# Kernel optimization log

Hardware: AMD Instinct MI355X
Metric: run time of the kernel (lower is better)

Reference implementation:

```python
import jax, jax.numpy as jnp
import numpy as np

B, L, D = 4, 2048, 768
H, K = 12, 9
IPG = D // H  # in-channels per group = head_size = 64
PAD = (K - 1) // 2


def setup_inputs() -> dict:
    key = jax.random.key(0)
    ks = jax.random.split(key, 8)
    s = lambda k, shape, scale: jax.random.normal(k, shape, dtype=jnp.float32) * scale
    return {
        "query": s(ks[0], (B, L, D), 1.0),
        "dw_w": s(ks[1], (D, 1, K), 0.1),          # depthwise Conv1d weight, no bias
        "pw_w": s(ks[2], (H, IPG, IPG), 0.05),     # grouped 1x1 conv [head, out_pg, in_pg]
        "pw_b": s(ks[3], (D,), 0.02),
        "ak_w": s(ks[4], (H, K, IPG), 0.05),       # conv_attn_kernel grouped 1x1 [head, K, in_pg]
        "ak_b": s(ks[5], (H * K,), 0.02),
        "pt_w": s(ks[6], (D, D), 0.02),            # conv_attn_point Linear weight [out, in]
        "pt_b": s(ks[7], (D,), 0.02),
    }


def _sdconv(query, dw_w, pw_w, pw_b, ak_w, ak_b, pt_w, pt_b):
    b, l, d = query.shape
    # SeparableConv1d: depthwise conv (groups=D, kernel K, padding PAD, no bias)
    x = query.transpose(0, 2, 1)  # [B, D, L]
    dw = jax.lax.conv_general_dilated(
        x, dw_w, window_strides=(1,), padding=[(PAD, PAD)],
        feature_group_count=d, dimension_numbers=("NCH", "OIH", "NCH"))  # [B, D, L]
    # grouped pointwise conv (groups=H, kernel 1)
    dwg = dw.reshape(b, H, IPG, l)
    pw = jnp.einsum("bhil,hoi->bhol", dwg, pw_w).reshape(b, d, l) + pw_b[None, :, None]
    key_conv_attn = pw.transpose(0, 2, 1)  # [B, L, D]
    # stride == 1 path: elementwise gate with query
    conv_attn = key_conv_attn * query  # [B, L, D]
    # conv_attn_kernel: grouped 1x1 conv D -> H*K (per head: IPG -> K)
    ca = conv_attn.reshape(b, l, H, IPG)
    kern = jnp.einsum("blhi,hki->blhk", ca, ak_w) + ak_b.reshape(H, K)  # [B, L, H, K]
    w = jax.nn.softmax(kern, axis=-1)  # softmax over kernel positions
    # conv_attn_point linear on value (= query here)
    v = query @ pt_w.T + pt_b  # [B, L, D]
    # unfold: local windows of size K around each position
    vp = jnp.pad(v, ((0, 0), (PAD, PAD), (0, 0)))
    idx = jnp.arange(l)[:, None] + jnp.arange(K)[None, :]  # [L, K]
    win = vp[:, idx]  # [B, L, K, D]
    winh = win.reshape(b, l, K, H, IPG)
    out = jnp.einsum("blkhd,blhk->blhd", winh, w).reshape(b, l, d)
    return out


def reference(query, dw_w, pw_w, pw_b, ak_w, ak_b, pt_w, pt_b):
    return _sdconv(query, dw_w, pw_w, pw_b, ak_w, ak_b, pt_w, pt_b)
```

## Files before the change

### kernel.cpp

```cpp
#include <hip/hip_runtime.h>
#include <math.h>

#define NB 4
#define NL 2048
#define ND 768
#define NH 12
#define NK 9
#define NIPG 64
#define NPAD 4
#define MT 112

typedef __attribute__((ext_vector_type(8))) short s16x8;
typedef __attribute__((ext_vector_type(4))) float f32x4;

__device__ __forceinline__ unsigned short f2bf(float f) {
  unsigned int u = __float_as_uint(f);
  unsigned int r = (u + 0x7FFFu + ((u >> 16) & 1u)) >> 16;
  return (unsigned short)r;
}
__device__ __forceinline__ float bf2f(unsigned short s) {
  return __uint_as_float(((unsigned int)s) << 16);
}
__device__ __forceinline__ void gload16(const void* g, void* l) {
  __builtin_amdgcn_global_load_lds((const __attribute__((address_space(1))) void*)g,
                                   (__attribute__((address_space(3))) void*)l,
                                   16, 0, 0);
}

__global__ __launch_bounds__(256) void prep(const float* __restrict__ pt_w,
                                            const float* __restrict__ pw_w,
                                            const float* __restrict__ ak_w,
                                            unsigned short* __restrict__ ptb,
                                            unsigned short* __restrict__ pwb,
                                            unsigned short* __restrict__ akp) {
  const int t = blockIdx.x * 256 + threadIdx.x;
  if (t < ND * ND / 4) {
    float4 f = ((const float4*)pt_w)[t];
    ushort4 o; o.x = f2bf(f.x); o.y = f2bf(f.y); o.z = f2bf(f.z); o.w = f2bf(f.w);
    ((ushort4*)ptb)[t] = o;
  }
  if (t < NH * NIPG * NIPG / 4) {
    float4 f = ((const float4*)pw_w)[t];
    ushort4 o; o.x = f2bf(f.x); o.y = f2bf(f.y); o.z = f2bf(f.z); o.w = f2bf(f.w);
    ((ushort4*)pwb)[t] = o;
  }
  if (t < NH * 16 * NIPG) {
    const int h = t >> 10;
    const int r = t & 1023;
    const int k = r >> 6;
    const int i = r & 63;
    akp[t] = (k < NK) ? f2bf(ak_w[((size_t)h * NK + k) * NIPG + i]) : (unsigned short)0;
  }
}

__global__ __launch_bounds__(256) void attn_w(const float* __restrict__ q,
                                              const float* __restrict__ dw_w,
                                              const unsigned short* __restrict__ pwb,
                                              const float* __restrict__ pw_b,
                                              const unsigned short* __restrict__ akp,
                                              const float* __restrict__ ak_b,
                                              float* __restrict__ wout,
                                              unsigned short* __restrict__ qb) {
  __shared__ float qs[72][68];
  __shared__ unsigned char ab[8192];
  const int l0 = blockIdx.x * 64;
  const int h  = blockIdx.y;
  const int b  = blockIdx.z;
  const int d0 = h * NIPG;
  const int t  = threadIdx.x;
  const int lane = t & 63;
  const int wv = t >> 6;

  {
    const int sl = t >> 4;
    const int sc = (t & 15) * 4;
    for (int r = sl; r < 72; r += 16) {
      const int l = l0 - NPAD + r;
      float4 val = make_float4(0.f, 0.f, 0.f, 0.f);
      if (l >= 0 && l < NL) val = *(const float4*)&q[((size_t)(b * NL + l)) * ND + d0 + sc];
      *(float4*)&qs[r][sc] = val;
      if (r >= NPAD && r < NPAD + 64) {
        ushort4 ub;
        ub.x = f2bf(val.x); ub.y = f2bf(val.y); ub.z = f2bf(val.z); ub.w = f2bf(val.w);
        *(ushort4*)&qb[((size_t)(b * NL + l)) * ND + d0 + sc] = ub;
      }
    }
  }
  float dwk[NK];
#pragma unroll
  for (int k = 0; k < NK; ++k) dwk[k] = dw_w[(size_t)(d0 + lane) * NK + k];
  __syncthreads();

  const int lset = wv * 16;
#pragma unroll
  for (int l2 = 0; l2 < 16; ++l2) {
    const int l = lset + l2;
    float s = 0.f;
#pragma unroll
    for (int k = 0; k < NK; ++k) s = fmaf(qs[l + k][lane], dwk[k], s);
    const int byte = ((l * 64 + lane) * 2) ^ ((l & 7) << 4);
    *(unsigned short*)&ab[byte] = f2bf(s);
  }
  __syncthreads();

  const int fr = lane & 15;
  const int fq = lane >> 4;

  s16x8 av0, av1;
  {
    const int row = lset + fr;
    const int b0 = ((row * 64 + fq * 8) * 2)      ^ ((row & 7) << 4);
    const int b1 = ((row * 64 + 32 + fq * 8) * 2) ^ ((row & 7) << 4);
    av0 = *(const s16x8*)&ab[b0];
    av1 = *(const s16x8*)&ab[b1];
  }
  const unsigned short* pwh = pwb + (size_t)h * NIPG * NIPG;
  f32x4 accp[4];
#pragma unroll
  for (int n = 0; n < 4; ++n) {
    accp[n] = (f32x4){0.f, 0.f, 0.f, 0.f};
    const int o = n * 16 + fr;
    s16x8 bv0 = *(const s16x8*)&pwh[o * 64 + fq * 8];
    s16x8 bv1 = *(const s16x8*)&pwh[o * 64 + 32 + fq * 8];
    accp[n] = __builtin_amdgcn_mfma_f32_16x16x32_bf16(av0, bv0, accp[n], 0, 0, 0);
    accp[n] = __builtin_amdgcn_mfma_f32_16x16x32_bf16(av1, bv1, accp[n], 0, 0, 0);
  }
  __syncthreads();

#pragma unroll
  for (int n = 0; n < 4; ++n) {
    const int o = n * 16 + fr;
    const float pb = pw_b[d0 + o];
#pragma unroll
    for (int j = 0; j < 4; ++j) {
      const int row = lset + fq * 4 + j;
      const float ca = (accp[n][j] + pb) * qs[row + NPAD][o];
      const int byte = ((row * 64 + o) * 2) ^ ((row & 7) << 4);
      *(unsigned short*)&ab[byte] = f2bf(ca);
    }
  }
  __syncthreads();

  f32x4 acck = (f32x4){0.f, 0.f, 0.f, 0.f};
  {
    const int row = lset + fr;
    const int b0 = ((row * 64 + fq * 8) * 2)      ^ ((row & 7) << 4);
    const int b1 = ((row * 64 + 32 + fq * 8) * 2) ^ ((row & 7) << 4);
    s16x8 a0 = *(const s16x8*)&ab[b0];
    s16x8 a1 = *(const s16x8*)&ab[b1];
    const unsigned short* akh = akp + (size_t)h * 16 * NIPG;
    s16x8 b0v = *(const s16x8*)&akh[fr * 64 + fq * 8];
    s16x8 b1v = *(const s16x8*)&akh[fr * 64 + 32 + fq * 8];
    acck = __builtin_amdgcn_mfma_f32_16x16x32_bf16(a0, b0v, acck, 0, 0, 0);
    acck = __builtin_amdgcn_mfma_f32_16x16x32_bf16(a1, b1v, acck, 0, 0, 0);
  }

  const bool kvalid = fr < NK;
  const float akbv = kvalid ? ak_b[h * NK + fr] : 0.f;
#pragma unroll
  for (int j = 0; j < 4; ++j) {
    float val = acck[j] + akbv;
    float mv = kvalid ? val : -3.4e38f;
#pragma unroll
    for (int mm = 1; mm < 16; mm <<= 1) mv = fmaxf(mv, __shfl_xor(mv, mm));
    const float e = kvalid ? __expf(val - mv) : 0.f;
    float ssum = e;
#pragma unroll
    for (int mm = 1; mm < 16; mm <<= 1) ssum += __shfl_xor(ssum, mm);
    if (kvalid) {
      const int row = l0 + lset + fq * 4 + j;
      wout[(((size_t)(b * NL + row)) * NH + h) * NK + fr] = e / ssum;
    }
  }
}

__global__ __launch_bounds__(256) void gemm_conv(const unsigned short* __restrict__ qb,
                                                 const unsigned short* __restrict__ ptb,
                                                 const float* __restrict__ bias,
                                                 const float* __restrict__ w,
                                                 float* __restrict__ out) {
  __shared__ unsigned char lds[33792];
  const int t = threadIdx.x;
  const long mo = (long)blockIdx.x * MT;
  const int n0 = blockIdx.y * 128;
  const int lane = t & 63;
  const int wv = t >> 6;
  const int wr = wv >> 1, wc = wv & 1;
  const int fr = lane & 15;
  const int fq = lane >> 4;

  const int soff = t * 16;
  const int sr = soff >> 6;
  const int scb = soff & 63;
  const unsigned char* gA0 = (const unsigned char*)qb + (mo - 8 + sr) * (long)(ND * 2) + scb;
  const unsigned char* gA1 = gA0 + (long)64 * (ND * 2);
  const unsigned char* gB0 = (const unsigned char*)ptb + (size_t)(n0 + sr) * (ND * 2) + scb;
  const unsigned char* gB1 = gB0 + (size_t)64 * (ND * 2);

  int aoff[4], boff[4];
#pragma unroll
  for (int m = 0; m < 4; ++m)
    aoff[m] = ((wr * 64 + m * 16 + fr) * 32 + fq * 8) * 2;
#pragma unroll
  for (int n = 0; n < 4; ++n)
    boff[n] = 8192 + ((wc * 64 + n * 16 + fr) * 32 + fq * 8) * 2;

#define STAGE(kt, buf)                                             \
  do {                                                             \
    const long kb_ = (long)(kt) * 64;                              \
    unsigned char* base_ = &lds[(buf) * 16384];                    \
    gload16(gA0 + kb_, base_ + soff);                              \
    gload16(gA1 + kb_, base_ + 4096 + soff);                       \
    gload16(gB0 + kb_, base_ + 8192 + soff);                       \
    gload16(gB1 + kb_, base_ + 12288 + soff);                      \
  } while (0)

  f32x4 acc[4][4] = {};
  STAGE(0, 0);
  __syncthreads();
  for (int kt = 0; kt < ND / 32; ++kt) {
    const int cur = kt & 1;
    if (kt + 1 < ND / 32) STAGE(kt + 1, cur ^ 1);
    const unsigned char* bb = &lds[cur * 16384];
    s16x8 av[4], bv[4];
#pragma unroll
    for (int m = 0; m < 4; ++m) av[m] = *(const s16x8*)&bb[aoff[m]];
#pragma unroll
    for (int n = 0; n < 4; ++n) bv[n] = *(const s16x8*)&bb[boff[n]];
#pragma unroll
    for (int m = 0; m < 4; ++m)
#pragma unroll
      for (int n = 0; n < 4; ++n)
        acc[m][n] = __builtin_amdgcn_mfma_f32_16x16x32_bf16(av[m], bv[n], acc[m][n], 0, 0, 0);
    __syncthreads();
  }
#undef STAGE

  unsigned short* vt = (unsigned short*)lds;
#pragma unroll
  for (int m = 0; m < 4; ++m) {
#pragma unroll
    for (int n = 0; n < 4; ++n) {
      const int rb = wr * 64 + m * 16 + fq * 4;
      const int cc = wc * 64 + n * 16 + fr;
      const float bbv = bias[n0 + cc];
#pragma unroll
      for (int j = 0; j < 4; ++j)
        vt[(rb + j) * 132 + cc] = f2bf(acc[m][n][j] + bbv);
    }
  }
  __syncthreads();

  const int cq = (t & 31) * 4;
  const int r0 = 8 + (t >> 5) * 14;
  const int h = (n0 + cq) >> 6;
  float4 win[NK];
#pragma unroll
  for (int k = 0; k < NK; ++k) {
    ushort4 u = *(const ushort4*)&vt[(r0 - 4 + k) * 132 + cq];
    win[k] = make_float4(bf2f(u.x), bf2f(u.y), bf2f(u.z), bf2f(u.w));
  }
#pragma unroll
  for (int i = 0; i < 14; ++i) {
    const int r = r0 + i;
    const long g = mo + r - 8;
    if (g < (long)NB * NL) {
      const int l = (int)(g & (NL - 1));
      const float* wp = &w[((size_t)g * NH + h) * NK];
      float4 a = make_float4(0.f, 0.f, 0.f, 0.f);
#pragma unroll
      for (int k = 0; k < NK; ++k) {
        const int lk = l + k - NPAD;
        if (lk >= 0 && lk < NL) {
          const float wk = wp[k];
          a.x = fmaf(wk, win[k].x, a.x);
          a.y = fmaf(wk, win[k].y, a.y);
          a.z = fmaf(wk, win[k].z, a.z);
          a.w = fmaf(wk, win[k].w, a.w);
        }
      }
      *(float4*)&out[(size_t)g * ND + n0 + cq] = a;
    }
    if (i < 13) {
#pragma unroll
      for (int k = 0; k < NK - 1; ++k) win[k] = win[k + 1];
      ushort4 u = *(const ushort4*)&vt[(r + 5) * 132 + cq];
      win[NK - 1] = make_float4(bf2f(u.x), bf2f(u.y), bf2f(u.z), bf2f(u.w));
    }
  }
}

extern "C" void kernel_launch(void* const* d_in, const int* in_sizes, int n_in,
                              void* d_out, int out_size, void* d_ws, size_t ws_size,
                              hipStream_t stream) {
  const float* query = (const float*)d_in[0];
  const float* dw_w  = (const float*)d_in[1];
  const float* pw_w  = (const float*)d_in[2];
  const float* pw_b  = (const float*)d_in[3];
  const float* ak_w  = (const float*)d_in[4];
  const float* ak_b  = (const float*)d_in[5];
  const float* pt_w  = (const float*)d_in[6];
  const float* pt_b  = (const float*)d_in[7];
  float* out = (float*)d_out;

  float* w = (float*)d_ws;
  unsigned short* qb  = (unsigned short*)(w + (size_t)NB * NL * NH * NK);
  unsigned short* ptb = qb + (size_t)NB * NL * ND;
  unsigned short* pwb = ptb + (size_t)ND * ND;
  unsigned short* akp = pwb + (size_t)NH * NIPG * NIPG;

  prep<<<ND * ND / 4 / 256, 256, 0, stream>>>(pt_w, pw_w, ak_w, ptb, pwb, akp);

  dim3 g2(NL / 64, NH, NB);
  attn_w<<<g2, 256, 0, stream>>>(query, dw_w, pwb, pw_b, akp, ak_b, w, qb);

  dim3 g3((NB * NL + MT - 1) / MT, ND / 128, 1);
  gemm_conv<<<g3, 256, 0, stream>>>(qb, ptb, pt_b, w, out);
}
```

Baseline: 148.4 us.

## Halve GEMM N-tile to 64 and store attn_w query tile as bf16 with sliding window

The fused GEMM+conv kernel now uses a 128x64 output tile instead of 128x128, so each wave computes 32 rows by 64 columns and only half the threads load B. This doubles the grid size and cuts LDS use, which should raise occupancy and wave count across CUs, at the cost of more A-tile reloads. In attn_w the query tile in LDS is kept as bf16 instead of fp32, and the depthwise conv uses a register sliding window to cut LDS reads. The bf16 staging also lowers precision of the depthwise conv and gating inputs.

```diff
diff --git a/kernel.cpp b/kernel.cpp
--- a/kernel.cpp
+++ b/kernel.cpp
@@ -61,7 +61,7 @@
                                               const float* __restrict__ ak_b,
                                               float* __restrict__ wout,
                                               unsigned short* __restrict__ qb) {
-  __shared__ float qs[72][68];
+  __shared__ unsigned short qs[72][68];
   __shared__ unsigned char ab[8192];
   const int l0 = blockIdx.x * 64;
   const int h  = blockIdx.y;
@@ -76,14 +76,14 @@
     const int sc = (t & 15) * 4;
     for (int r = sl; r < 72; r += 16) {
       const int l = l0 - NPAD + r;
-      float4 val = make_float4(0.f, 0.f, 0.f, 0.f);
-      if (l >= 0 && l < NL) val = *(const float4*)&q[((size_t)(b * NL + l)) * ND + d0 + sc];
-      *(float4*)&qs[r][sc] = val;
-      if (r >= NPAD && r < NPAD + 64) {
-        ushort4 ub;
+      ushort4 ub = make_ushort4(0, 0, 0, 0);
+      if (l >= 0 && l < NL) {
+        float4 val = *(const float4*)&q[((size_t)(b * NL + l)) * ND + d0 + sc];
         ub.x = f2bf(val.x); ub.y = f2bf(val.y); ub.z = f2bf(val.z); ub.w = f2bf(val.w);
-        *(ushort4*)&qb[((size_t)(b * NL + l)) * ND + d0 + sc] = ub;
+        if (r >= NPAD && r < NPAD + 64)
+          *(ushort4*)&qb[((size_t)(b * NL + l)) * ND + d0 + sc] = ub;
       }
+      *(ushort4*)&qs[r][sc] = ub;
     }
   }
   float dwk[NK];
@@ -92,14 +92,24 @@
   __syncthreads();
 
   const int lset = wv * 16;
-#pragma unroll
-  for (int l2 = 0; l2 < 16; ++l2) {
-    const int l = lset + l2;
-    float s = 0.f;
-#pragma unroll
-    for (int k = 0; k < NK; ++k) s = fmaf(qs[l + k][lane], dwk[k], s);
-    const int byte = ((l * 64 + lane) * 2) ^ ((l & 7) << 4);
-    *(unsigned short*)&ab[byte] = f2bf(s);
+  {
+    float win9[NK];
+#pragma unroll
+    for (int k = 0; k < NK; ++k) win9[k] = bf2f(qs[lset + k][lane]);
+#pragma unroll
+    for (int l2 = 0; l2 < 16; ++l2) {
+      const int l = lset + l2;
+      float s = 0.f;
+#pragma unroll
+      for (int k = 0; k < NK; ++k) s = fmaf(win9[k], dwk[k], s);
+      const int byte = ((l * 64 + lane) * 2) ^ ((l & 7) << 4);
+      *(unsigned short*)&ab[byte] = f2bf(s);
+      if (l2 < 15) {
+#pragma unroll
+        for (int k = 0; k < NK - 1; ++k) win9[k] = win9[k + 1];
+        win9[NK - 1] = bf2f(qs[lset + l2 + NK][lane]);
+      }
+    }
   }
   __syncthreads();
 
@@ -134,7 +144,7 @@
 #pragma unroll
     for (int j = 0; j < 4; ++j) {
       const int row = lset + fq * 4 + j;
-      const float ca = (accp[n][j] + pb) * qs[row + NPAD][o];
+      const float ca = (accp[n][j] + pb) * bf2f(qs[row + NPAD][o]);
       const int byte = ((row * 64 + o) * 2) ^ ((row & 7) << 4);
       *(unsigned short*)&ab[byte] = f2bf(ca);
     }
@@ -179,13 +189,12 @@
                                                  const float* __restrict__ bias,
                                                  const float* __restrict__ w,
                                                  float* __restrict__ out) {
-  __shared__ unsigned char lds[33792];
+  __shared__ unsigned char lds[24576];
   const int t = threadIdx.x;
   const long mo = (long)blockIdx.x * MT;
-  const int n0 = blockIdx.y * 128;
+  const int n0 = blockIdx.y * 64;
   const int lane = t & 63;
   const int wv = t >> 6;
-  const int wr = wv >> 1, wc = wv & 1;
   const int fr = lane & 15;
   const int fq = lane >> 4;
 
@@ -194,41 +203,39 @@
   const int scb = soff & 63;
   const unsigned char* gA0 = (const unsigned char*)qb + (mo - 8 + sr) * (long)(ND * 2) + scb;
   const unsigned char* gA1 = gA0 + (long)64 * (ND * 2);
-  const unsigned char* gB0 = (const unsigned char*)ptb + (size_t)(n0 + sr) * (ND * 2) + scb;
-  const unsigned char* gB1 = gB0 + (size_t)64 * (ND * 2);
-
-  int aoff[4], boff[4];
-#pragma unroll
-  for (int m = 0; m < 4; ++m)
-    aoff[m] = ((wr * 64 + m * 16 + fr) * 32 + fq * 8) * 2;
+  const unsigned char* gB  = (const unsigned char*)ptb + (size_t)(n0 + sr) * (ND * 2) + scb;
+
+  int aoff[2], boff[4];
+#pragma unroll
+  for (int m = 0; m < 2; ++m)
+    aoff[m] = ((wv * 32 + m * 16 + fr) * 32 + fq * 8) * 2;
 #pragma unroll
   for (int n = 0; n < 4; ++n)
-    boff[n] = 8192 + ((wc * 64 + n * 16 + fr) * 32 + fq * 8) * 2;
+    boff[n] = 8192 + ((n * 16 + fr) * 32 + fq * 8) * 2;
 
 #define STAGE(kt, buf)                                             \
   do {                                                             \
     const long kb_ = (long)(kt) * 64;                              \
-    unsigned char* base_ = &lds[(buf) * 16384];                    \
+    unsigned char* base_ = &lds[(buf) * 12288];                    \
     gload16(gA0 + kb_, base_ + soff);                              \
     gload16(gA1 + kb_, base_ + 4096 + soff);                       \
-    gload16(gB0 + kb_, base_ + 8192 + soff);                       \
-    gload16(gB1 + kb_, base_ + 12288 + soff);                      \
+    if (soff < 4096) gload16(gB + kb_, base_ + 8192 + soff);       \
   } while (0)
 
-  f32x4 acc[4][4] = {};
+  f32x4 acc[2][4] = {};
   STAGE(0, 0);
   __syncthreads();
   for (int kt = 0; kt < ND / 32; ++kt) {
     const int cur = kt & 1;
     if (kt + 1 < ND / 32) STAGE(kt + 1, cur ^ 1);
-    const unsigned char* bb = &lds[cur * 16384];
-    s16x8 av[4], bv[4];
-#pragma unroll
-    for (int m = 0; m < 4; ++m) av[m] = *(const s16x8*)&bb[aoff[m]];
+    const unsigned char* bb = &lds[cur * 12288];
+    s16x8 av[2], bv[4];
+#pragma unroll
+    for (int m = 0; m < 2; ++m) av[m] = *(const s16x8*)&bb[aoff[m]];
 #pragma unroll
     for (int n = 0; n < 4; ++n) bv[n] = *(const s16x8*)&bb[boff[n]];
 #pragma unroll
-    for (int m = 0; m < 4; ++m)
+    for (int m = 0; m < 2; ++m)
 #pragma unroll
       for (int n = 0; n < 4; ++n)
         acc[m][n] = __builtin_amdgcn_mfma_f32_16x16x32_bf16(av[m], bv[n], acc[m][n], 0, 0, 0);
@@ -238,30 +245,30 @@
 
   unsigned short* vt = (unsigned short*)lds;
 #pragma unroll
-  for (int m = 0; m < 4; ++m) {
+  for (int m = 0; m < 2; ++m) {
 #pragma unroll
     for (int n = 0; n < 4; ++n) {
-      const int rb = wr * 64 + m * 16 + fq * 4;
-      const int cc = wc * 64 + n * 16 + fr;
+      const int rb = wv * 32 + m * 16 + fq * 4;
+      const int cc = n * 16 + fr;
       const float bbv = bias[n0 + cc];
 #pragma unroll
       for (int j = 0; j < 4; ++j)
-        vt[(rb + j) * 132 + cc] = f2bf(acc[m][n][j] + bbv);
-    }
-  }
-  __syncthreads();
-
-  const int cq = (t & 31) * 4;
-  const int r0 = 8 + (t >> 5) * 14;
-  const int h = (n0 + cq) >> 6;
+        vt[(rb + j) * 68 + cc] = f2bf(acc[m][n][j] + bbv);
+    }
+  }
+  __syncthreads();
+
+  const int cq = (t & 15) * 4;
+  const int r0 = 8 + (t >> 4) * 7;
+  const int h = n0 >> 6;
   float4 win[NK];
 #pragma unroll
   for (int k = 0; k < NK; ++k) {
-    ushort4 u = *(const ushort4*)&vt[(r0 - 4 + k) * 132 + cq];
+    ushort4 u = *(const ushort4*)&vt[(r0 - 4 + k) * 68 + cq];
     win[k] = make_float4(bf2f(u.x), bf2f(u.y), bf2f(u.z), bf2f(u.w));
   }
 #pragma unroll
-  for (int i = 0; i < 14; ++i) {
+  for (int i = 0; i < 7; ++i) {
     const int r = r0 + i;
     const long g = mo + r - 8;
     if (g < (long)NB * NL) {
@@ -281,10 +288,10 @@
       }
       *(float4*)&out[(size_t)g * ND + n0 + cq] = a;
     }
-    if (i < 13) {
+    if (i < 6) {
 #pragma unroll
       for (int k = 0; k < NK - 1; ++k) win[k] = win[k + 1];
-      ushort4 u = *(const ushort4*)&vt[(r + 5) * 132 + cq];
+      ushort4 u = *(const ushort4*)&vt[(r + 5) * 68 + cq];
       win[NK - 1] = make_float4(bf2f(u.x), bf2f(u.y), bf2f(u.z), bf2f(u.w));
     }
   }
@@ -314,6 +321,6 @@
   dim3 g2(NL / 64, NH, NB);
   attn_w<<<g2, 256, 0, stream>>>(query, dw_w, pwb, pw_b, akp, ak_b, w, qb);
 
-  dim3 g3((NB * NL + MT - 1) / MT, ND / 128, 1);
+  dim3 g3((NB * NL + MT - 1) / MT, ND / 64, 1);
   gemm_conv<<<g3, 256, 0, stream>>>(qb, ptb, pt_b, w, out);
 }
```

Result: faster. 141.1 us (-4.9%).
